# Optimization experiments

Measured on AMD Instinct MI355X. Metric: run time of the kernel, lower is better.

## Reference

```python
import jax, jax.numpy as jnp
import numpy as np

EPS = 1e-5

def layer_norm(x, g, b):
    mu = jnp.mean(x, axis=-1, keepdims=True)
    var = jnp.mean((x - mu) ** 2, axis=-1, keepdims=True)
    return (x - mu) * jax.lax.rsqrt(var + EPS) * g + b

def setup_inputs() -> dict:
    key = jax.random.key(0)
    ks = jax.random.split(key, 13)
    B, N, C, H = 2, 2048, 1024, 16
    Dff = 4 * C
    s = lambda k, shape, fan_in: jax.random.normal(k, shape, jnp.float32) * (1.0 / np.sqrt(fan_in))
    return {
        "x": jax.random.normal(ks[0], (B, N, C), jnp.float32),
        "ln1_g": jnp.ones((C,), jnp.float32),
        "ln1_b": jnp.zeros((C,), jnp.float32),
        "qkv_w": s(ks[1], (3 * C, C), C),
        "qkv_b": jnp.zeros((3 * C,), jnp.float32),
        "proj_w": s(ks[2], (C, C), C),
        "proj_b": jnp.zeros((C,), jnp.float32),
        "ln2_g": jnp.ones((C,), jnp.float32),
        "ln2_b": jnp.zeros((C,), jnp.float32),
        "fc1_w": s(ks[3], (Dff, C), C),
        "fc1_b": jnp.zeros((Dff,), jnp.float32),
        "fc2_w": s(ks[4], (C, Dff), Dff),
        "fc2_b": jnp.zeros((C,), jnp.float32),
    }

def reference(x, ln1_g, ln1_b, qkv_w, qkv_b, proj_w, proj_b, ln2_g, ln2_b, fc1_w, fc1_b, fc2_w, fc2_b):
    B, N, C = x.shape
    H = 16
    D = C // H
    # --- attention sub-block (pre-norm) ---
    h = layer_norm(x, ln1_g, ln1_b)
    qkv = h @ qkv_w.T + qkv_b                      # [B,N,3C]
    qkv = qkv.reshape(B, N, 3, H, D).transpose(2, 0, 3, 1, 4)  # [3,B,H,N,D]
    q, k, v = qkv[0], qkv[1], qkv[2]
    attn = jnp.einsum('bhnd,bhmd->bhnm', q, k) * (D ** -0.5)   # [B,H,N,N]
    attn = jax.nn.softmax(attn, axis=-1)
    o = jnp.einsum('bhnm,bhmd->bhnd', attn, v)     # [B,H,N,D]
    o = o.transpose(0, 2, 1, 3).reshape(B, N, C)
    x = x + (o @ proj_w.T + proj_b)
    # --- MLP sub-block (pre-norm) ---
    h = layer_norm(x, ln2_g, ln2_b)
    h = jax.nn.gelu(h @ fc1_w.T + fc1_b, approximate=False)
    x = x + (h @ fc2_w.T + fc2_b)
    return x
```

## Files before the change

### kernel.cpp

```cpp
#include <hip/hip_runtime.h>
#include <hip/hip_bf16.h>
#include <math.h>

typedef __bf16 bf16;
typedef __bf16 bf16x8 __attribute__((ext_vector_type(8)));
typedef __bf16 bf16x4 __attribute__((ext_vector_type(4)));
typedef float  f32x4  __attribute__((ext_vector_type(4)));

typedef __attribute__((address_space(1))) void gvoid;
typedef __attribute__((address_space(3))) void lvoid;
#define GLOAD_LDS16(gp, lp) __builtin_amdgcn_global_load_lds((gvoid*)(gp), (lvoid*)(lp), 16, 0, 0)

__global__ __launch_bounds__(256) void prep(
    const float* __restrict__ qkvw, const float* __restrict__ projw,
    const float* __restrict__ fc1w, const float* __restrict__ fc2w,
    bf16* __restrict__ qkvw_h, bf16* __restrict__ projw_h,
    bf16* __restrict__ fc1w_h, bf16* __restrict__ fc2w_h,
    const float* __restrict__ x, const float* __restrict__ g,
    const float* __restrict__ b, bf16* __restrict__ h1) {
  int blk = blockIdx.x;
  if (blk < 12288) {
    const float* in; bf16* out; int base;
    if (blk < 3072)      { in = qkvw; out = qkvw_h; base = blk; }
    else if (blk < 4096) { in = projw; out = projw_h; base = blk - 3072; }
    else if (blk < 8192) { in = fc1w; out = fc1w_h; base = blk - 4096; }
    else                 { in = fc2w; out = fc2w_h; base = blk - 8192; }
    int i = (base * 256 + threadIdx.x) * 4;
    f32x4 v = *(const f32x4*)(in + i);
    bf16x4 o;
    #pragma unroll
    for (int e = 0; e < 4; ++e) o[e] = (bf16)v[e];
    *(bf16x4*)(out + i) = o;
    return;
  }
  int w = threadIdx.x >> 6, l = threadIdx.x & 63;
  size_t row = (size_t)(blk - 12288) * 4 + w;
  const float* xr = x + row * 1024;
  float f[16];
  #pragma unroll
  for (int c = 0; c < 4; ++c) {
    f32x4 v = *(const f32x4*)(xr + c * 256 + l * 4);
    #pragma unroll
    for (int e = 0; e < 4; ++e) f[c * 4 + e] = v[e];
  }
  float s = 0.f, ss = 0.f;
  #pragma unroll
  for (int e = 0; e < 16; ++e) { s += f[e]; ss += f[e] * f[e]; }
  #pragma unroll
  for (int d = 1; d < 64; d <<= 1) { s += __shfl_xor(s, d); ss += __shfl_xor(ss, d); }
  float mean = s * (1.f / 1024.f);
  float var  = ss * (1.f / 1024.f) - mean * mean;
  float rstd = rsqrtf(var + 1e-5f);
  #pragma unroll
  for (int c = 0; c < 4; ++c) {
    f32x4 gv = *(const f32x4*)(g + c * 256 + l * 4);
    f32x4 bv = *(const f32x4*)(b + c * 256 + l * 4);
    bf16x4 ov;
    #pragma unroll
    for (int e = 0; e < 4; ++e)
      ov[e] = (bf16)((f[c * 4 + e] - mean) * rstd * gv[e] + bv[e]);
    *(bf16x4*)(h1 + row * 1024 + c * 256 + l * 4) = ov;
  }
}

__global__ __launch_bounds__(256) void ln_f32(const float* __restrict__ x,
    const float* __restrict__ g, const float* __restrict__ b, bf16* __restrict__ out) {
  int w = threadIdx.x >> 6, l = threadIdx.x & 63;
  size_t row = (size_t)blockIdx.x * 4 + w;
  const float* xr = x + row * 1024;
  float f[16];
  #pragma unroll
  for (int c = 0; c < 4; ++c) {
    f32x4 v = *(const f32x4*)(xr + c * 256 + l * 4);
    #pragma unroll
    for (int e = 0; e < 4; ++e) f[c * 4 + e] = v[e];
  }
  float s = 0.f, ss = 0.f;
  #pragma unroll
  for (int e = 0; e < 16; ++e) { s += f[e]; ss += f[e] * f[e]; }
  #pragma unroll
  for (int d = 1; d < 64; d <<= 1) { s += __shfl_xor(s, d); ss += __shfl_xor(ss, d); }
  float mean = s * (1.f / 1024.f);
  float var  = ss * (1.f / 1024.f) - mean * mean;
  float rstd = rsqrtf(var + 1e-5f);
  #pragma unroll
  for (int c = 0; c < 4; ++c) {
    f32x4 gv = *(const f32x4*)(g + c * 256 + l * 4);
    f32x4 bv = *(const f32x4*)(b + c * 256 + l * 4);
    bf16x4 ov;
    #pragma unroll
    for (int e = 0; e < 4; ++e)
      ov[e] = (bf16)((f[c * 4 + e] - mean) * rstd * gv[e] + bv[e]);
    *(bf16x4*)(out + row * 1024 + c * 256 + l * 4) = ov;
  }
}

#define SWZ(tp) ((tp) ^ ((((tp) >> 9) & 1) << 5))
#define STAGE(buf, op, half, kt_) do { \
    const char* gp_ = (const char*)((op) ? Wp : Ap); \
    int t0_ = (op) ? colBase : rowBase; \
    const int P_ = (op) ? 12 : 13; \
    _Pragma("unroll") for (int s_ = 0; s_ < 2; ++s_) { \
      int b14_ = w * 2048 + s_ * 1024; \
      int tb_ = ((b14_ >> P_) << (P_ + 1)) | ((half) << P_) | (b14_ & ((1 << P_) - 1)); \
      int tq_ = SWZ(tb_ + l * 16); \
      GLOAD_LDS16(gp_ + ((size_t)(t0_ + (tq_ >> 7)) * lda + (size_t)(kt_) * 64) * 2 + (tq_ & 127), \
                  smbase + (buf) * 65536 + (op) * 32768 + tb_); \
    } \
  } while (0)
#define LDA(buf, mi, kk) (*(const bf16x8*)(smbase + (buf) * 65536 + \
    SWZ((wm * 128 + (mi) * 16 + lr) * 128 + (kk) * 64 + lg * 16)))
#define LDB(buf, ni, kk) (*(const bf16x8*)(smbase + (buf) * 65536 + 32768 + \
    SWZ((wn * 64 + (ni) * 16 + lr) * 128 + (kk) * 64 + lg * 16)))
#define RD_A(buf, MI0) { _Pragma("unroll") for (int i_ = 0; i_ < 4; ++i_) \
    _Pragma("unroll") for (int k_ = 0; k_ < 2; ++k_) a[i_][k_] = LDA(buf, (MI0) + i_, k_); }
#define RD_B(buf, NI0) { _Pragma("unroll") for (int j_ = 0; j_ < 2; ++j_) \
    _Pragma("unroll") for (int k_ = 0; k_ < 2; ++k_) bq[j_][k_] = LDB(buf, (NI0) + j_, k_); }
#define MFMA16(MI0, NI0) do { __builtin_amdgcn_s_setprio(1); \
    _Pragma("unroll") for (int i_ = 0; i_ < 4; ++i_) \
    _Pragma("unroll") for (int j_ = 0; j_ < 2; ++j_) \
    _Pragma("unroll") for (int k_ = 0; k_ < 2; ++k_) \
      acc[(MI0) + i_][(NI0) + j_] = __builtin_amdgcn_mfma_f32_16x16x32_bf16( \
          a[i_][k_], bq[j_][k_], acc[(MI0) + i_][(NI0) + j_], 0, 0, 0); \
    __builtin_amdgcn_s_setprio(0); } while (0)
#define BARX() __builtin_amdgcn_s_barrier()
#define LGK0() asm volatile("s_waitcnt lgkmcnt(0)")
#define VM4()  asm volatile("s_waitcnt vmcnt(4)")

template<int ACT, int HASBIAS, typename TO>
__global__ __launch_bounds__(512, 2) void gemm256(const bf16* __restrict__ Ap,
    const bf16* __restrict__ Wp, const float* __restrict__ bias,
    TO* __restrict__ out, int lda, int N, int klen, int nbx, size_t outSlice) {
  __shared__ bf16 smem_[2][2][256 * 64];
  char* smbase = (char*)smem_;
  int tid = threadIdx.x, w = tid >> 6, l = tid & 63, lr = l & 15, lg = l >> 4;
  int wm = w >> 2, wn = w & 3;
  int q = gridDim.x >> 3;
  int wg = ((int)blockIdx.x & 7) * q + ((int)blockIdx.x >> 3);
  int rowBase = (wg / nbx) * 256, colBase = (wg % nbx) * 256;
  Ap += (size_t)blockIdx.y * klen;
  Wp += (size_t)blockIdx.y * klen;
  out += (size_t)blockIdx.y * outSlice;

  f32x4 acc[8][4];
  const f32x4 fz = {0.f, 0.f, 0.f, 0.f};
  #pragma unroll
  for (int i = 0; i < 8; ++i)
    #pragma unroll
    for (int j = 0; j < 4; ++j) acc[i][j] = fz;
  bf16x8 a[4][2], bq[2][2];
  int nkt = klen >> 6;

  STAGE(0, 0, 0, 0); STAGE(0, 1, 0, 0); STAGE(0, 0, 1, 0); STAGE(0, 1, 1, 0);
  STAGE(1, 1, 0, 1); STAGE(1, 0, 1, 1);
  VM4(); BARX();

  for (int t = 0; t < nkt; t += 2) {
    int t1 = t + 1;
    int t2 = t + 2 < nkt ? t + 2 : nkt - 1;
    int t3 = t + 3 < nkt ? t + 3 : nkt - 1;
    RD_A(0, 0); RD_B(0, 0);
    STAGE(1, 0, 0, t1); STAGE(1, 1, 1, t1);
    BARX(); LGK0(); MFMA16(0, 0); BARX();
    RD_A(0, 4);
    BARX(); LGK0(); MFMA16(4, 0); BARX();
    RD_B(0, 2);
    STAGE(0, 1, 0, t2);
    BARX(); LGK0(); MFMA16(4, 2); BARX();
    RD_A(0, 0);
    STAGE(0, 0, 1, t2);
    VM4();
    BARX(); LGK0(); MFMA16(0, 2); BARX();
    RD_A(1, 0); RD_B(1, 0);
    STAGE(0, 0, 0, t2); STAGE(0, 1, 1, t2);
    BARX(); LGK0(); MFMA16(0, 0); BARX();
    RD_A(1, 4);
    BARX(); LGK0(); MFMA16(4, 0); BARX();
    RD_B(1, 2);
    STAGE(1, 1, 0, t3);
    BARX(); LGK0(); MFMA16(4, 2); BARX();
    RD_A(1, 0);
    STAGE(1, 0, 1, t3);
    VM4();
    BARX(); LGK0(); MFMA16(0, 2); BARX();
  }

  #pragma unroll
  for (int ni = 0; ni < 4; ++ni) {
    int col = colBase + wn * 64 + ni * 16 + lr;
    float bv = HASBIAS ? bias[col] : 0.f;
    #pragma unroll
    for (int mi = 0; mi < 8; ++mi) {
      #pragma unroll
      for (int jj = 0; jj < 4; ++jj) {
        int row2 = rowBase + wm * 128 + mi * 16 + lg * 4 + jj;
        float v = acc[mi][ni][jj] + bv;
        if constexpr (ACT == 1) v = 0.5f * v * (1.f + erff(v * 0.70710678118f));
        out[(size_t)row2 * N + col] = (TO)v;
      }
    }
  }
}

__global__ __launch_bounds__(256) void projred_ln(const bf16* __restrict__ part,
    const float* __restrict__ x, const float* __restrict__ pb,
    const float* __restrict__ g, const float* __restrict__ bb,
    float* __restrict__ x1, bf16* __restrict__ h2) {
  int w = threadIdx.x >> 6, l = threadIdx.x & 63;
  size_t row = (size_t)blockIdx.x * 4 + w;
  size_t rb = row * 1024;
  float f[16];
  #pragma unroll
  for (int c = 0; c < 4; ++c) {
    int off = c * 256 + l * 4;
    f32x4 v = *(const f32x4*)(x + rb + off);
    v += *(const f32x4*)(pb + off);
    #pragma unroll
    for (int sl = 0; sl < 4; ++sl) {
      bf16x4 pv = *(const bf16x4*)(part + (size_t)sl * 4194304 + rb + off);
      #pragma unroll
      for (int e = 0; e < 4; ++e) v[e] += (float)pv[e];
    }
    *(f32x4*)(x1 + rb + off) = v;
    #pragma unroll
    for (int e = 0; e < 4; ++e) f[c * 4 + e] = v[e];
  }
  float s = 0.f, ss = 0.f;
  #pragma unroll
  for (int e = 0; e < 16; ++e) { s += f[e]; ss += f[e] * f[e]; }
  #pragma unroll
  for (int d = 1; d < 64; d <<= 1) { s += __shfl_xor(s, d); ss += __shfl_xor(ss, d); }
  float mean = s * (1.f / 1024.f);
  float var  = ss * (1.f / 1024.f) - mean * mean;
  float rstd = rsqrtf(var + 1e-5f);
  #pragma unroll
  for (int c = 0; c < 4; ++c) {
    int off = c * 256 + l * 4;
    f32x4 gv = *(const f32x4*)(g + off);
    f32x4 bv = *(const f32x4*)(bb + off);
    bf16x4 ov;
    #pragma unroll
    for (int e = 0; e < 4; ++e)
      ov[e] = (bf16)((f[c * 4 + e] - mean) * rstd * gv[e] + bv[e]);
    *(bf16x4*)(h2 + rb + off) = ov;
  }
}

__global__ __launch_bounds__(256) void fc2_red(const bf16* __restrict__ part,
    const float* __restrict__ x1, const float* __restrict__ bias,
    float* __restrict__ out) {
  int i = (blockIdx.x * 256 + threadIdx.x) * 4;
  f32x4 s = *(const f32x4*)(x1 + i);
  s += *(const f32x4*)(bias + (i & 1023));
  #pragma unroll
  for (int k = 0; k < 4; ++k) {
    bf16x4 pv = *(const bf16x4*)(part + (size_t)k * 4194304 + i);
    #pragma unroll
    for (int e = 0; e < 4; ++e) s[e] += (float)pv[e];
  }
  *(f32x4*)(out + i) = s;
}

template<int ACT, int HASRES, typename TO>
__global__ __launch_bounds__(256) void gemm_bt(const bf16* __restrict__ A,
    const bf16* __restrict__ W, const float* __restrict__ bias,
    const float* __restrict__ res, TO* __restrict__ out, int M, int N, int K) {
  __shared__ bf16 As[128 * 32];
  __shared__ bf16 Bs[128 * 32];
  int tid = threadIdx.x;
  int w = tid >> 6, l = tid & 63;
  int lr = l & 15, lg = l >> 4;
  int wm = w >> 1, wn = w & 1;
  int rowBase = blockIdx.y * 128;
  int colBase = blockIdx.x * 128;
  f32x4 acc[4][4];
  const f32x4 fz = {0.f, 0.f, 0.f, 0.f};
  #pragma unroll
  for (int i = 0; i < 4; ++i)
    #pragma unroll
    for (int j = 0; j < 4; ++j) acc[i][j] = fz;
  for (int kt = 0; kt < K; kt += 32) {
    __syncthreads();
    #pragma unroll
    for (int j = 0; j < 2; ++j) {
      int u = (w * 2 + j) * 64 + l;
      int r = u >> 2, cb = (u & 3) * 8;
      GLOAD_LDS16(A + (size_t)(rowBase + r) * K + kt + cb, As + (w * 2 + j) * 512);
      GLOAD_LDS16(W + (size_t)(colBase + r) * K + kt + cb, Bs + (w * 2 + j) * 512);
    }
    __syncthreads();
    bf16x8 af[4], bfr[4];
    #pragma unroll
    for (int mi = 0; mi < 4; ++mi)
      af[mi] = *(const bf16x8*)(As + (wm * 64 + mi * 16 + lr) * 32 + lg * 8);
    #pragma unroll
    for (int ni = 0; ni < 4; ++ni)
      bfr[ni] = *(const bf16x8*)(Bs + (wn * 64 + ni * 16 + lr) * 32 + lg * 8);
    #pragma unroll
    for (int mi = 0; mi < 4; ++mi)
      #pragma unroll
      for (int ni = 0; ni < 4; ++ni)
        acc[mi][ni] = __builtin_amdgcn_mfma_f32_16x16x32_bf16(af[mi], bfr[ni], acc[mi][ni], 0, 0, 0);
  }
  #pragma unroll
  for (int ni = 0; ni < 4; ++ni) {
    int col = colBase + wn * 64 + ni * 16 + lr;
    float bv = bias[col];
    #pragma unroll
    for (int mi = 0; mi < 4; ++mi) {
      #pragma unroll
      for (int jj = 0; jj < 4; ++jj) {
        int row2 = rowBase + wm * 64 + mi * 16 + lg * 4 + jj;
        float v = acc[mi][ni][jj] + bv;
        if constexpr (ACT == 1) v = 0.5f * v * (1.f + erff(v * 0.70710678118f));
        if constexpr (HASRES)   v += res[(size_t)row2 * N + col];
        out[(size_t)row2 * N + col] = (TO)v;
      }
    }
  }
}

__global__ __launch_bounds__(256) void attn_kernel(const bf16* __restrict__ qkv,
                                                   bf16* __restrict__ o) {
  const int Nn = 2048, C3 = 3072;
  int tid = threadIdx.x, w = tid >> 6, l = tid & 63, lr = l & 15, lg = l >> 4;
  int lin = blockIdx.x;
  int wg = (lin & 7) * 128 + (lin >> 3);
  int qb = wg & 31, bh = wg >> 5;
  int b = bh >> 4, h = bh & 15;
  size_t hb = (size_t)b * Nn * C3 + h * 64;
  const bf16* Qp = qkv + hb;
  __shared__ bf16 Ks[2][64 * 64];
  __shared__ bf16 Vt[2][64 * 64];
  __shared__ bf16 Ps[4][16 * 64];

  int q0 = qb * 64 + w * 16;
  bf16x8 qf[2];
  #pragma unroll
  for (int kk = 0; kk < 2; ++kk) {
    bf16x8 t = *(const bf16x8*)(Qp + (size_t)(q0 + lr) * C3 + kk * 32 + lg * 8);
    #pragma unroll
    for (int e = 0; e < 8; ++e) qf[kk][e] = (bf16)((float)t[e] * 0.18033688f);
  }

  int sz = (lr & 7) << 4;
  int s45 = (lr & 3) << 4, s6 = (lr & 4) << 4;
  int l2 = l * 2;
  int kr0 = tid >> 3, c80 = (tid & 7) * 8;
  char* ksw = (char*)Ks + kr0 * 128 + ((c80 * 2) ^ ((kr0 & 7) << 4));
  char* vtw = (char*)Vt + w * 1024;
  const char* ksr0 = (const char*)Ks + lr * 128 + ((lg * 16) ^ sz);
  const char* ksr1 = (const char*)Ks + lr * 128 + (((64) + lg * 16) ^ sz);
  const char* vtrA = (const char*)Vt + lr * 128 + ((lg * 16) ^ s45) + s6;
  const char* vtrB = (const char*)Vt + lr * 128 + ((lg * 16) ^ s45) + (64 ^ s6);
  char* psb = (char*)Ps[w] + lr * 128;
  char* psw0 = psb + ((lg * 8) ^ sz);
  char* psw1 = psb + ((32 + lg * 8) ^ sz);
  char* psw2 = psb + ((64 + lg * 8) ^ sz);
  char* psw3 = psb + ((96 + lg * 8) ^ sz);
  const char* psr0 = psb + ((lg * 16) ^ sz);
  const char* psr1 = psb + ((64 + lg * 16) ^ sz);

  const bf16* kp0 = qkv + hb + 1024 + (size_t)kr0 * C3 + c80;
  const bf16* kp1 = kp0 + (size_t)32 * C3;
  const bf16* vp0 = qkv + hb + 2048 + (size_t)l * C3 + w * 8;
  const int step = 64 * C3;

  const f32x4 fz = {0.f, 0.f, 0.f, 0.f};
  f32x4 oa[4];
  #pragma unroll
  for (int c = 0; c < 4; ++c) oa[c] = fz;
  float mrow = -1e30f, srow = 0.f;

  bf16x8 kg0 = *(const bf16x8*)kp0; kp0 += step;
  bf16x8 kg1 = *(const bf16x8*)kp1; kp1 += step;
  bf16x8 vg0 = *(const bf16x8*)vp0;
  bf16x8 vg1 = *(const bf16x8*)(vp0 + 32); vp0 += step;
  *(bf16x8*)(ksw) = kg0;
  *(bf16x8*)(ksw + 4096) = kg1;
  #pragma unroll
  for (int e = 0; e < 8; ++e) {
    *(bf16*)(vtw + e * 128 + (l2 ^ (e << 4)))        = vg0[e];
    *(bf16*)(vtw + 4096 + e * 128 + (l2 ^ (e << 4))) = vg1[e];
  }
  __syncthreads();

  for (int t = 0; t < 32; ++t) {
    int bo = (t & 1) << 13;
    if (t < 31) {
      kg0 = *(const bf16x8*)kp0; kp0 += step;
      kg1 = *(const bf16x8*)kp1; kp1 += step;
      vg0 = *(const bf16x8*)vp0;
      vg1 = *(const bf16x8*)(vp0 + 32); vp0 += step;
    }

    f32x4 sc[4];
    __builtin_amdgcn_s_setprio(1);
    #pragma unroll
    for (int c = 0; c < 4; ++c) {
      f32x4 acm = fz;
      acm = __builtin_amdgcn_mfma_f32_16x16x32_bf16(
          *(const bf16x8*)(ksr0 + bo + c * 2048), qf[0], acm, 0, 0, 0);
      acm = __builtin_amdgcn_mfma_f32_16x16x32_bf16(
          *(const bf16x8*)(ksr1 + bo + c * 2048), qf[1], acm, 0, 0, 0);
      sc[c] = acm;
    }
    __builtin_amdgcn_s_setprio(0);

    float m0 = fmaxf(fmaxf(sc[0][0], sc[0][1]), fmaxf(sc[0][2], sc[0][3]));
    float m1 = fmaxf(fmaxf(sc[1][0], sc[1][1]), fmaxf(sc[1][2], sc[1][3]));
    float m2 = fmaxf(fmaxf(sc[2][0], sc[2][1]), fmaxf(sc[2][2], sc[2][3]));
    float m3 = fmaxf(fmaxf(sc[3][0], sc[3][1]), fmaxf(sc[3][2], sc[3][3]));
    float mt = fmaxf(fmaxf(m0, m1), fmaxf(m2, m3));
    mt = fmaxf(mt, __shfl_xor(mt, 16));
    mt = fmaxf(mt, __shfl_xor(mt, 32));
    if (!__all(mt - mrow <= 8.f)) {
      float mn = fmaxf(mrow, mt);
      float al = exp2f(mrow - mn);
      mrow = mn;
      srow *= al;
      #pragma unroll
      for (int c = 0; c < 4; ++c)
        #pragma unroll
        for (int j = 0; j < 4; ++j) oa[c][j] *= al;
    }
    float p[4][4];
    float rs = 0.f;
    #pragma unroll
    for (int c = 0; c < 4; ++c) {
      float r0 = exp2f(sc[c][0] - mrow), r1 = exp2f(sc[c][1] - mrow);
      float r2 = exp2f(sc[c][2] - mrow), r3 = exp2f(sc[c][3] - mrow);
      p[c][0] = r0; p[c][1] = r1; p[c][2] = r2; p[c][3] = r3;
      rs += (r0 + r1) + (r2 + r3);
    }
    rs += __shfl_xor(rs, 16);
    rs += __shfl_xor(rs, 32);
    srow += rs;

    bf16x4 pk0, pk1, pk2, pk3;
    #pragma unroll
    for (int j = 0; j < 4; ++j) {
      pk0[j] = (bf16)p[0][j]; pk1[j] = (bf16)p[1][j];
      pk2[j] = (bf16)p[2][j]; pk3[j] = (bf16)p[3][j];
    }
    *(bf16x4*)psw0 = pk0; *(bf16x4*)psw1 = pk1;
    *(bf16x4*)psw2 = pk2; *(bf16x4*)psw3 = pk3;
    bf16x8 pb0 = *(const bf16x8*)psr0;
    bf16x8 pb1 = *(const bf16x8*)psr1;
    __builtin_amdgcn_s_setprio(1);
    #pragma unroll
    for (int cd = 0; cd < 4; ++cd) {
      oa[cd] = __builtin_amdgcn_mfma_f32_16x16x32_bf16(
          *(const bf16x8*)(vtrA + bo + cd * 2048), pb0, oa[cd], 0, 0, 0);
      oa[cd] = __builtin_amdgcn_mfma_f32_16x16x32_bf16(
          *(const bf16x8*)(vtrB + bo + cd * 2048), pb1, oa[cd], 0, 0, 0);
    }
    __builtin_amdgcn_s_setprio(0);

    if (t < 31) {
      int bo2 = bo ^ 8192;
      *(bf16x8*)(ksw + bo2) = kg0;
      *(bf16x8*)(ksw + 4096 + bo2) = kg1;
      #pragma unroll
      for (int e = 0; e < 8; ++e) {
        *(bf16*)(vtw + bo2 + e * 128 + (l2 ^ (e << 4)))        = vg0[e];
        *(bf16*)(vtw + bo2 + 4096 + e * 128 + (l2 ^ (e << 4))) = vg1[e];
      }
      __syncthreads();
    }
  }

  float inv = 1.f / srow;
  size_t qr = (size_t)q0 + lr;
  #pragma unroll
  for (int cd = 0; cd < 4; ++cd)
    #pragma unroll
    for (int j = 0; j < 4; ++j)
      o[((size_t)b * Nn + qr) * 1024 + h * 64 + cd * 16 + lg * 4 + j] =
          (bf16)(oa[cd][j] * inv);
}

extern "C" void kernel_launch(void* const* d_in, const int* in_sizes, int n_in,
                              void* d_out, int out_size, void* d_ws, size_t ws_size,
                              hipStream_t stream) {
  (void)in_sizes; (void)n_in; (void)out_size;
  const float* x     = (const float*)d_in[0];
  const float* ln1g  = (const float*)d_in[1];
  const float* ln1b  = (const float*)d_in[2];
  const float* qkvw  = (const float*)d_in[3];
  const float* qkvb  = (const float*)d_in[4];
  const float* projw = (const float*)d_in[5];
  const float* projb = (const float*)d_in[6];
  const float* ln2g  = (const float*)d_in[7];
  const float* ln2b  = (const float*)d_in[8];
  const float* fc1w  = (const float*)d_in[9];
  const float* fc1b  = (const float*)d_in[10];
  const float* fc2w  = (const float*)d_in[11];
  const float* fc2b  = (const float*)d_in[12];

  char* ws = (char*)d_ws;
  bf16*  qkvw_h = (bf16*)(ws);
  bf16*  projw_h= (bf16*)(ws + (6ull  << 20));
  bf16*  fc1w_h = (bf16*)(ws + (8ull  << 20));
  bf16*  fc2w_h = (bf16*)(ws + (16ull << 20));
  bf16*  h1     = (bf16*)(ws + (24ull << 20));
  bf16*  qkv    = (bf16*)(ws + (32ull << 20));
  bf16*  ov     = (bf16*)(ws + (64ull << 20));
  float* x1     = (float*)(ws + (72ull << 20));
  bf16*  parts  = (bf16*)(ws + (96ull << 20));
  bf16*  h2  = h1;
  bf16*  ffn = qkv;
  bool big = ws_size >= (160ull << 20);

  const int M = 4096;
  prep<<<dim3(12288 + 1024), 256, 0, stream>>>(qkvw, projw, fc1w, fc2w,
      qkvw_h, projw_h, fc1w_h, fc2w_h, x, ln1g, ln1b, h1);
  gemm256<0, 1, bf16><<<dim3(192), dim3(512), 0, stream>>>(
      h1, qkvw_h, qkvb, qkv, 1024, 3072, 1024, 12, 0);
  attn_kernel<<<dim3(1024), 256, 0, stream>>>(qkv, ov);
  if (big) {
    gemm256<0, 0, bf16><<<dim3(64, 4), dim3(512), 0, stream>>>(
        ov, projw_h, nullptr, parts, 1024, 1024, 256, 4, 4194304ull);
    projred_ln<<<dim3(1024), 256, 0, stream>>>(parts, x, projb, ln2g, ln2b, x1, h2);
  } else {
    gemm_bt<0, 1, float><<<dim3(8, 32), 256, 0, stream>>>(
        ov, projw_h, projb, x, x1, M, 1024, 1024);
    ln_f32<<<dim3(1024), 256, 0, stream>>>(x1, ln2g, ln2b, h2);
  }
  gemm256<1, 1, bf16><<<dim3(256), dim3(512), 0, stream>>>(
      h2, fc1w_h, fc1b, ffn, 1024, 4096, 1024, 16, 0);
  if (big) {
    gemm256<0, 0, bf16><<<dim3(64, 4), dim3(512), 0, stream>>>(
        ffn, fc2w_h, nullptr, parts, 4096, 1024, 1024, 4, 4194304ull);
    fc2_red<<<dim3(4096), 256, 0, stream>>>(parts, x1, fc2b, (float*)d_out);
  } else {
    gemm_bt<0, 1, float><<<dim3(8, 32), 256, 0, stream>>>(
        ffn, fc2w_h, fc2b, x1, (float*)d_out, M, 1024, 4096);
  }
}
```

Baseline: 281.0 us.

## Rewrite attention with 32x32x16 MFMA and register-resident P fragments

```diff
diff --git a/kernel.cpp b/kernel.cpp
--- a/kernel.cpp
+++ b/kernel.cpp
@@ -6,6 +6,8 @@
 typedef __bf16 bf16x8 __attribute__((ext_vector_type(8)));
 typedef __bf16 bf16x4 __attribute__((ext_vector_type(4)));
 typedef float  f32x4  __attribute__((ext_vector_type(4)));
+typedef float  f32x16 __attribute__((ext_vector_type(16)));
+typedef int    i32x4  __attribute__((ext_vector_type(4)));
 
 typedef __attribute__((address_space(1))) void gvoid;
 typedef __attribute__((address_space(3))) void lvoid;
@@ -320,56 +322,64 @@
   }
 }
 
+#define MKFRAG(S, T, OUT) do { \
+    int a_, b_, c_, d_; \
+    asm("v_cvt_pk_bf16_f32 %0, %1, %2" : "=v"(a_) : "v"((S)[8*(T)+0]), "v"((S)[8*(T)+1])); \
+    asm("v_cvt_pk_bf16_f32 %0, %1, %2" : "=v"(b_) : "v"((S)[8*(T)+4]), "v"((S)[8*(T)+5])); \
+    asm("v_cvt_pk_bf16_f32 %0, %1, %2" : "=v"(c_) : "v"((S)[8*(T)+2]), "v"((S)[8*(T)+3])); \
+    asm("v_cvt_pk_bf16_f32 %0, %1, %2" : "=v"(d_) : "v"((S)[8*(T)+6]), "v"((S)[8*(T)+7])); \
+    asm("v_permlane32_swap_b32 %0, %1" : "+v"(a_), "+v"(b_)); \
+    asm("v_permlane32_swap_b32 %0, %1" : "+v"(c_), "+v"(d_)); \
+    i32x4 wv_ = {a_, c_, b_, d_}; \
+    OUT = __builtin_bit_cast(bf16x8, wv_); \
+  } while (0)
+
 __global__ __launch_bounds__(256) void attn_kernel(const bf16* __restrict__ qkv,
                                                    bf16* __restrict__ o) {
   const int Nn = 2048, C3 = 3072;
-  int tid = threadIdx.x, w = tid >> 6, l = tid & 63, lr = l & 15, lg = l >> 4;
+  int tid = threadIdx.x, w = tid >> 6, l = tid & 63;
+  int q32 = l & 31, hi = l >> 5, hi4 = hi * 4;
   int lin = blockIdx.x;
-  int wg = (lin & 7) * 128 + (lin >> 3);
-  int qb = wg & 31, bh = wg >> 5;
+  int wg = (lin & 7) * 64 + (lin >> 3);
+  int qb = wg & 15, bh = wg >> 4;
   int b = bh >> 4, h = bh & 15;
   size_t hb = (size_t)b * Nn * C3 + h * 64;
   const bf16* Qp = qkv + hb;
   __shared__ bf16 Ks[2][64 * 64];
   __shared__ bf16 Vt[2][64 * 64];
-  __shared__ bf16 Ps[4][16 * 64];
-
-  int q0 = qb * 64 + w * 16;
-  bf16x8 qf[2];
-  #pragma unroll
-  for (int kk = 0; kk < 2; ++kk) {
-    bf16x8 t = *(const bf16x8*)(Qp + (size_t)(q0 + lr) * C3 + kk * 32 + lg * 8);
-    #pragma unroll
-    for (int e = 0; e < 8; ++e) qf[kk][e] = (bf16)((float)t[e] * 0.18033688f);
-  }
-
-  int sz = (lr & 7) << 4;
-  int s45 = (lr & 3) << 4, s6 = (lr & 4) << 4;
-  int l2 = l * 2;
+
+  int q0w = qb * 128 + w * 32;
+  bf16x8 qf[4];
+  {
+    const bf16* qrow = Qp + (size_t)(q0w + q32) * C3 + 8 * hi;
+    #pragma unroll
+    for (int dk = 0; dk < 4; ++dk) {
+      bf16x8 t = *(const bf16x8*)(qrow + 16 * dk);
+      #pragma unroll
+      for (int e = 0; e < 8; ++e) qf[dk][e] = (bf16)((float)t[e] * 0.18033688f);
+    }
+  }
+
+  int swz = (l & 7) << 4;
   int kr0 = tid >> 3, c80 = (tid & 7) * 8;
   char* ksw = (char*)Ks + kr0 * 128 + ((c80 * 2) ^ ((kr0 & 7) << 4));
   char* vtw = (char*)Vt + w * 1024;
-  const char* ksr0 = (const char*)Ks + lr * 128 + ((lg * 16) ^ sz);
-  const char* ksr1 = (const char*)Ks + lr * 128 + (((64) + lg * 16) ^ sz);
-  const char* vtrA = (const char*)Vt + lr * 128 + ((lg * 16) ^ s45) + s6;
-  const char* vtrB = (const char*)Vt + lr * 128 + ((lg * 16) ^ s45) + (64 ^ s6);
-  char* psb = (char*)Ps[w] + lr * 128;
-  char* psw0 = psb + ((lg * 8) ^ sz);
-  char* psw1 = psb + ((32 + lg * 8) ^ sz);
-  char* psw2 = psb + ((64 + lg * 8) ^ sz);
-  char* psw3 = psb + ((96 + lg * 8) ^ sz);
-  const char* psr0 = psb + ((lg * 16) ^ sz);
-  const char* psr1 = psb + ((64 + lg * 16) ^ sz);
+  int l2 = l * 2;
+  const char* abase = (const char*)Ks + q32 * 128;
+  const char* vbase = (const char*)Vt + q32 * 128;
+  int doff[4];
+  #pragma unroll
+  for (int dk = 0; dk < 4; ++dk) doff[dk] = (32 * dk + 16 * hi) ^ swz;
 
   const bf16* kp0 = qkv + hb + 1024 + (size_t)kr0 * C3 + c80;
   const bf16* kp1 = kp0 + (size_t)32 * C3;
   const bf16* vp0 = qkv + hb + 2048 + (size_t)l * C3 + w * 8;
   const int step = 64 * C3;
 
-  const f32x4 fz = {0.f, 0.f, 0.f, 0.f};
-  f32x4 oa[4];
-  #pragma unroll
-  for (int c = 0; c < 4; ++c) oa[c] = fz;
+  f32x16 zz;
+  #pragma unroll
+  for (int i = 0; i < 16; ++i) zz[i] = 0.f;
+  f32x16 oa0 = zz, oa1 = zz;
   float mrow = -1e30f, srow = 0.f;
 
   bf16x8 kg0 = *(const bf16x8*)kp0; kp0 += step;
@@ -394,25 +404,26 @@
       vg1 = *(const bf16x8*)(vp0 + 32); vp0 += step;
     }
 
-    f32x4 sc[4];
+    bf16x8 ka[2][4];
+    #pragma unroll
+    for (int kb = 0; kb < 2; ++kb)
+      #pragma unroll
+      for (int dk = 0; dk < 4; ++dk)
+        ka[kb][dk] = *(const bf16x8*)(abase + bo + kb * 4096 + doff[dk]);
+    f32x16 sc0 = zz, sc1 = zz;
     __builtin_amdgcn_s_setprio(1);
     #pragma unroll
-    for (int c = 0; c < 4; ++c) {
-      f32x4 acm = fz;
-      acm = __builtin_amdgcn_mfma_f32_16x16x32_bf16(
-          *(const bf16x8*)(ksr0 + bo + c * 2048), qf[0], acm, 0, 0, 0);
-      acm = __builtin_amdgcn_mfma_f32_16x16x32_bf16(
-          *(const bf16x8*)(ksr1 + bo + c * 2048), qf[1], acm, 0, 0, 0);
-      sc[c] = acm;
+    for (int dk = 0; dk < 4; ++dk) {
+      sc0 = __builtin_amdgcn_mfma_f32_32x32x16_bf16(ka[0][dk], qf[dk], sc0, 0, 0, 0);
+      sc1 = __builtin_amdgcn_mfma_f32_32x32x16_bf16(ka[1][dk], qf[dk], sc1, 0, 0, 0);
     }
     __builtin_amdgcn_s_setprio(0);
 
-    float m0 = fmaxf(fmaxf(sc[0][0], sc[0][1]), fmaxf(sc[0][2], sc[0][3]));
-    float m1 = fmaxf(fmaxf(sc[1][0], sc[1][1]), fmaxf(sc[1][2], sc[1][3]));
-    float m2 = fmaxf(fmaxf(sc[2][0], sc[2][1]), fmaxf(sc[2][2], sc[2][3]));
-    float m3 = fmaxf(fmaxf(sc[3][0], sc[3][1]), fmaxf(sc[3][2], sc[3][3]));
-    float mt = fmaxf(fmaxf(m0, m1), fmaxf(m2, m3));
-    mt = fmaxf(mt, __shfl_xor(mt, 16));
+    float mt = sc0[0];
+    #pragma unroll
+    for (int r = 1; r < 16; ++r) mt = fmaxf(mt, sc0[r]);
+    #pragma unroll
+    for (int r = 0; r < 16; ++r) mt = fmaxf(mt, sc1[r]);
     mt = fmaxf(mt, __shfl_xor(mt, 32));
     if (!__all(mt - mrow <= 8.f)) {
       float mn = fmaxf(mrow, mt);
@@ -420,41 +431,39 @@
       mrow = mn;
       srow *= al;
       #pragma unroll
-      for (int c = 0; c < 4; ++c)
-        #pragma unroll
-        for (int j = 0; j < 4; ++j) oa[c][j] *= al;
-    }
-    float p[4][4];
+      for (int r = 0; r < 16; ++r) {
+        float alr = __shfl(al, ((r & 3) + 8 * (r >> 2)) + hi4);
+        oa0[r] *= alr; oa1[r] *= alr;
+      }
+    }
     float rs = 0.f;
     #pragma unroll
-    for (int c = 0; c < 4; ++c) {
-      float r0 = exp2f(sc[c][0] - mrow), r1 = exp2f(sc[c][1] - mrow);
-      float r2 = exp2f(sc[c][2] - mrow), r3 = exp2f(sc[c][3] - mrow);
-      p[c][0] = r0; p[c][1] = r1; p[c][2] = r2; p[c][3] = r3;
-      rs += (r0 + r1) + (r2 + r3);
-    }
-    rs += __shfl_xor(rs, 16);
+    for (int r = 0; r < 16; ++r) { sc0[r] = exp2f(sc0[r] - mrow); rs += sc0[r]; }
+    #pragma unroll
+    for (int r = 0; r < 16; ++r) { sc1[r] = exp2f(sc1[r] - mrow); rs += sc1[r]; }
     rs += __shfl_xor(rs, 32);
     srow += rs;
 
-    bf16x4 pk0, pk1, pk2, pk3;
-    #pragma unroll
-    for (int j = 0; j < 4; ++j) {
-      pk0[j] = (bf16)p[0][j]; pk1[j] = (bf16)p[1][j];
-      pk2[j] = (bf16)p[2][j]; pk3[j] = (bf16)p[3][j];
-    }
-    *(bf16x4*)psw0 = pk0; *(bf16x4*)psw1 = pk1;
-    *(bf16x4*)psw2 = pk2; *(bf16x4*)psw3 = pk3;
-    bf16x8 pb0 = *(const bf16x8*)psr0;
-    bf16x8 pb1 = *(const bf16x8*)psr1;
+    bf16x8 pa0, pa1, pa2, pa3;
+    MKFRAG(sc0, 0, pa0);
+    MKFRAG(sc0, 1, pa1);
+    MKFRAG(sc1, 0, pa2);
+    MKFRAG(sc1, 1, pa3);
+    bf16x8 vb[2][4];
+    #pragma unroll
+    for (int db = 0; db < 2; ++db)
+      #pragma unroll
+      for (int ks = 0; ks < 4; ++ks)
+        vb[db][ks] = *(const bf16x8*)(vbase + bo + db * 4096 + ((32 * ks + 16 * hi) ^ swz));
     __builtin_amdgcn_s_setprio(1);
-    #pragma unroll
-    for (int cd = 0; cd < 4; ++cd) {
-      oa[cd] = __builtin_amdgcn_mfma_f32_16x16x32_bf16(
-          *(const bf16x8*)(vtrA + bo + cd * 2048), pb0, oa[cd], 0, 0, 0);
-      oa[cd] = __builtin_amdgcn_mfma_f32_16x16x32_bf16(
-          *(const bf16x8*)(vtrB + bo + cd * 2048), pb1, oa[cd], 0, 0, 0);
-    }
+    oa0 = __builtin_amdgcn_mfma_f32_32x32x16_bf16(pa0, vb[0][0], oa0, 0, 0, 0);
+    oa0 = __builtin_amdgcn_mfma_f32_32x32x16_bf16(pa1, vb[0][1], oa0, 0, 0, 0);
+    oa0 = __builtin_amdgcn_mfma_f32_32x32x16_bf16(pa2, vb[0][2], oa0, 0, 0, 0);
+    oa0 = __builtin_amdgcn_mfma_f32_32x32x16_bf16(pa3, vb[0][3], oa0, 0, 0, 0);
+    oa1 = __builtin_amdgcn_mfma_f32_32x32x16_bf16(pa0, vb[1][0], oa1, 0, 0, 0);
+    oa1 = __builtin_amdgcn_mfma_f32_32x32x16_bf16(pa1, vb[1][1], oa1, 0, 0, 0);
+    oa1 = __builtin_amdgcn_mfma_f32_32x32x16_bf16(pa2, vb[1][2], oa1, 0, 0, 0);
+    oa1 = __builtin_amdgcn_mfma_f32_32x32x16_bf16(pa3, vb[1][3], oa1, 0, 0, 0);
     __builtin_amdgcn_s_setprio(0);
 
     if (t < 31) {
@@ -471,13 +480,14 @@
   }
 
   float inv = 1.f / srow;
-  size_t qr = (size_t)q0 + lr;
-  #pragma unroll
-  for (int cd = 0; cd < 4; ++cd)
-    #pragma unroll
-    for (int j = 0; j < 4; ++j)
-      o[((size_t)b * Nn + qr) * 1024 + h * 64 + cd * 16 + lg * 4 + j] =
-          (bf16)(oa[cd][j] * inv);
+  bf16* ob = o + ((size_t)b * Nn + q0w + hi4) * 1024 + h * 64 + q32;
+  #pragma unroll
+  for (int r = 0; r < 16; ++r) {
+    const int cr = (r & 3) + 8 * (r >> 2);
+    float invr = __shfl(inv, cr + hi4);
+    ob[(size_t)cr * 1024]      = (bf16)(oa0[r] * invr);
+    ob[(size_t)cr * 1024 + 32] = (bf16)(oa1[r] * invr);
+  }
 }
 
 extern "C" void kernel_launch(void* const* d_in, const int* in_sizes, int n_in,
@@ -517,7 +527,7 @@
       qkvw_h, projw_h, fc1w_h, fc2w_h, x, ln1g, ln1b, h1);
   gemm256<0, 1, bf16><<<dim3(192), dim3(512), 0, stream>>>(
       h1, qkvw_h, qkvb, qkv, 1024, 3072, 1024, 12, 0);
-  attn_kernel<<<dim3(1024), 256, 0, stream>>>(qkv, ov);
+  attn_kernel<<<dim3(512), 256, 0, stream>>>(qkv, ov);
   if (big) {
     gemm256<0, 0, bf16><<<dim3(64, 4), dim3(512), 0, stream>>>(
         ov, projw_h, nullptr, parts, 1024, 1024, 256, 4, 4194304ull);
```

Measured after the change: 266.7 us. 1.05x faster.
